# Optimization experiments

Hardware: AMD Instinct MI355X
Metric: run time of the kernel (lower is better)

Reference implementation:

```python
import jax, jax.numpy as jnp
import numpy as np

PAD_IDX = 1
BATCH = 16
TLEN = 128
SLEN = 400          # full source length
AGENDA_LEN = 100    # slen_ in src_map
CONTEXT_LEN = SLEN - AGENDA_LEN
INPUT_SIZE = 1024
VOCAB = 32000
CVOCAB = 120


def setup_inputs() -> dict:
    key = jax.random.key(0)
    k1, k2, k3, k4, k5, k6, k7 = jax.random.split(key, 7)
    N = BATCH * TLEN
    hidden = jax.random.normal(k1, (N, INPUT_SIZE), dtype=jnp.float32)
    attn = jax.random.uniform(k2, (N, SLEN), dtype=jnp.float32)
    attn = attn / jnp.sum(attn, axis=1, keepdims=True)  # attention-like rows
    src_map = jax.random.uniform(k3, (AGENDA_LEN, BATCH, CVOCAB), dtype=jnp.float32)
    W = jax.random.normal(k4, (VOCAB, INPUT_SIZE), dtype=jnp.float32) * 0.02
    b = jnp.zeros((VOCAB,), dtype=jnp.float32)
    W_copy = jax.random.normal(k5, (1, INPUT_SIZE), dtype=jnp.float32) * 0.02
    b_copy = jnp.zeros((1,), dtype=jnp.float32)
    return {"hidden": hidden, "attn": attn, "src_map": src_map,
            "W": W, "b": b, "W_copy": W_copy, "b_copy": b_copy}


def reference(hidden, attn, src_map, W, b, W_copy, b_copy):
    # hidden: (tlen*batch, d), attn: (tlen*batch, slen), src_map: (agenda, batch, cvocab)
    agenda_len, batch, cvocab = src_map.shape
    slen = attn.shape[1]
    context_len = slen - agenda_len

    logits = hidden @ W.T + b                       # (N, vocab)
    logits = logits.at[:, PAD_IDX].set(-jnp.inf)
    prob = jax.nn.softmax(logits, axis=1)
    p_copy = jax.nn.sigmoid(hidden @ W_copy.T + b_copy)  # (N, 1)

    out_prob = prob * (1.0 - p_copy)                # (N, vocab)
    mul_attn = attn[:, context_len:] * p_copy       # (N, agenda)

    # rows are ordered (tlen, batch); bmm against per-batch indicator map
    ma = mul_attn.reshape(-1, batch, agenda_len)    # (tlen, batch, agenda)
    copy_prob = jnp.einsum('tba,abv->tbv', ma, src_map)  # (tlen, batch, cvocab)
    copy_prob = copy_prob.reshape(-1, cvocab)       # (N, cvocab)

    return jnp.concatenate([out_prob, copy_prob], axis=1), p_copy
```

## Files before the change

kernel.cpp:

```cpp
#include <hip/hip_runtime.h>

#define M_DIM 2048
#define K_DIM 1024
#define N_DIM 32000
#define CVOCAB 120
#define AGENDA 100
#define SLEN 400
#define CTX 300
#define BATCH 16
#define OUT_STRIDE 32120
#define PAD_IDX 1

#define TM 256
#define TN 256
#define BK 64

typedef float f32x4_t  __attribute__((ext_vector_type(4)));
typedef __bf16 bf16x8_t __attribute__((ext_vector_type(8)));
typedef unsigned short u16x8_t __attribute__((ext_vector_type(8)));
typedef unsigned short u16x4_t __attribute__((ext_vector_type(4)));

__device__ __forceinline__ unsigned short f2bf(float f) {
    union { float f; unsigned int u; } c; c.f = f;
    unsigned int u = c.u;
    u += 0x7FFFu + ((u >> 16) & 1u);
    return (unsigned short)(u >> 16);
}

__device__ __forceinline__ void async_copy16(const void* gsrc, void* ldst) {
    __builtin_amdgcn_global_load_lds(
        (__attribute__((address_space(1))) unsigned int*)(gsrc),
        (__attribute__((address_space(3))) unsigned int*)(ldst),
        16, 0, 0);
}

__global__ void cast_bf16_kernel(const float4* __restrict__ W, const float4* __restrict__ H,
                                 unsigned short* __restrict__ Wb, unsigned short* __restrict__ Hb) {
    const size_t NW4 = (size_t)N_DIM * K_DIM / 4;
    const size_t NH4 = (size_t)M_DIM * K_DIM / 4;
    size_t idx = (size_t)blockIdx.x * 256 + threadIdx.x;
    float4 v; unsigned short* dst;
    if (idx < NW4)            { v = W[idx];        dst = Wb + idx * 4; }
    else if (idx < NW4 + NH4) { v = H[idx - NW4];  dst = Hb + (idx - NW4) * 4; }
    else return;
    u16x4_t o;
    o[0] = f2bf(v.x); o[1] = f2bf(v.y); o[2] = f2bf(v.z); o[3] = f2bf(v.w);
    *(u16x4_t*)dst = o;
}

__global__ void pcopy_kernel(const float* __restrict__ hidden, const float* __restrict__ Wc,
                             const float* __restrict__ bc, float* __restrict__ pcopy) {
    int row  = blockIdx.x * 4 + (threadIdx.x >> 6);
    int lane = threadIdx.x & 63;
    const float4* h = (const float4*)(hidden + (size_t)row * K_DIM);
    const float4* w = (const float4*)Wc;
    float s = 0.f;
    #pragma unroll
    for (int i = 0; i < 4; ++i) {
        float4 a = h[lane + 64 * i];
        float4 b = w[lane + 64 * i];
        s += a.x * b.x + a.y * b.y + a.z * b.z + a.w * b.w;
    }
    #pragma unroll
    for (int m = 1; m < 64; m <<= 1) s += __shfl_xor(s, m);
    if (lane == 0) {
        float p = 1.0f / (1.0f + __expf(-(s + bc[0])));
        pcopy[row] = p;
    }
}

__global__ __launch_bounds__(1024, 4) void gemm_exp_kernel(
    const unsigned short* __restrict__ A,
    const unsigned short* __restrict__ B,
    const float* __restrict__ bias,
    float* __restrict__ out,
    float* __restrict__ rowsum)
{
    __shared__ unsigned short sA[TM * BK];
    __shared__ unsigned short sB[TN * BK];
    __shared__ float sRow[TM];

    const int tid   = threadIdx.x;
    const int lane  = tid & 63;
    const int q     = lane >> 4;
    const int lr    = lane & 15;
    const int wv    = tid >> 6;
    const int waveM = wv >> 2;
    const int waveN = wv & 3;
    const int rowBase = blockIdx.x * TM;
    const int colBase = blockIdx.y * TN;

    f32x4_t acc[4][4] = {};

    if (tid < TM) sRow[tid] = 0.0f;

    const unsigned short* aSrc[2];
    const unsigned short* bSrc[2];
    unsigned short* aDst[2];
    unsigned short* bDst[2];
    #pragma unroll
    for (int it = 0; it < 2; ++it) {
        int p = it * 1024 + tid;
        int m = p >> 3;
        int j = (p & 7) ^ (m & 7);
        aSrc[it] = A + (size_t)(rowBase + m) * K_DIM + j * 8;
        bSrc[it] = B + (size_t)(colBase + m) * K_DIM + j * 8;
        aDst[it] = sA + (it * 1024 + (tid & ~63)) * 8;
        bDst[it] = sB + (it * 1024 + (tid & ~63)) * 8;
    }

    for (int k0 = 0; k0 < K_DIM; k0 += BK) {
        #pragma unroll
        for (int it = 0; it < 2; ++it) async_copy16(aSrc[it] + k0, aDst[it]);
        #pragma unroll
        for (int it = 0; it < 2; ++it) async_copy16(bSrc[it] + k0, bDst[it]);
        __syncthreads();

        #pragma unroll
        for (int s = 0; s < 2; ++s) {
            u16x8_t af[4], bfr[4];
            #pragma unroll
            for (int r = 0; r < 4; ++r) {
                int m  = waveM * 64 + r * 16 + lr;
                int ch = (s * 4 + q) ^ (m & 7);
                af[r] = *(const u16x8_t*)(sA + m * BK + ch * 8);
            }
            #pragma unroll
            for (int c = 0; c < 4; ++c) {
                int n  = waveN * 64 + c * 16 + lr;
                int ch = (s * 4 + q) ^ (n & 7);
                bfr[c] = *(const u16x8_t*)(sB + n * BK + ch * 8);
            }
            #pragma unroll
            for (int r = 0; r < 4; ++r)
                #pragma unroll
                for (int c = 0; c < 4; ++c)
                    acc[r][c] = __builtin_amdgcn_mfma_f32_16x16x32_bf16(
                        __builtin_bit_cast(bf16x8_t, af[r]),
                        __builtin_bit_cast(bf16x8_t, bfr[c]),
                        acc[r][c], 0, 0, 0);
        }
        __syncthreads();
    }

    float bb[4];
    #pragma unroll
    for (int c = 0; c < 4; ++c) bb[c] = bias[colBase + waveN * 64 + c * 16 + lr];

    #pragma unroll
    for (int r = 0; r < 4; ++r) {
        float rsum[4] = {0.f, 0.f, 0.f, 0.f};
        #pragma unroll
        for (int c = 0; c < 4; ++c) {
            int gcol = colBase + waveN * 64 + c * 16 + lr;
            #pragma unroll
            for (int d = 0; d < 4; ++d) {
                int grow = rowBase + waveM * 64 + r * 16 + q * 4 + d;
                float e = (gcol == PAD_IDX) ? 0.0f : __expf(acc[r][c][d] + bb[c]);
                out[(size_t)grow * OUT_STRIDE + gcol] = e;
                rsum[d] += e;
            }
        }
        #pragma unroll
        for (int d = 0; d < 4; ++d) {
            float v = rsum[d];
            v += __shfl_xor(v, 1);
            v += __shfl_xor(v, 2);
            v += __shfl_xor(v, 4);
            v += __shfl_xor(v, 8);
            if (lr == 0) {
                int lrow = waveM * 64 + r * 16 + q * 4 + d;
                atomicAdd(&sRow[lrow], v);
            }
        }
    }
    __syncthreads();
    if (tid < TM) atomicAdd(&rowsum[rowBase + tid], sRow[tid]);
}

__global__ void finalize_kernel(float* __restrict__ out, const float* __restrict__ rowsum,
                                const float* __restrict__ pcopy, const float* __restrict__ attn,
                                const float* __restrict__ src_map, float* __restrict__ out_tail) {
    int n   = blockIdx.x;
    int tid = threadIdx.x;
    int bidx = n & (BATCH - 1);
    float p = pcopy[n];
    float scale = (1.0f - p) / rowsum[n];

    __shared__ float ma[AGENDA];
    if (tid < AGENDA) ma[tid] = attn[(size_t)n * SLEN + CTX + tid] * p;

    float4* row4 = (float4*)(out + (size_t)n * OUT_STRIDE);
    for (int j = tid; j < N_DIM / 4; j += 256) {
        float4 v = row4[j];
        v.x *= scale; v.y *= scale; v.z *= scale; v.w *= scale;
        row4[j] = v;
    }
    __syncthreads();

    if (tid < CVOCAB) {
        float s = 0.f;
        #pragma unroll 4
        for (int a = 0; a < AGENDA; ++a)
            s += ma[a] * src_map[(size_t)(a * BATCH + bidx) * CVOCAB + tid];
        out[(size_t)n * OUT_STRIDE + N_DIM + tid] = s;
    }
    if (tid == 0) out_tail[n] = p;
}

extern "C" void kernel_launch(void* const* d_in, const int* in_sizes, int n_in,
                              void* d_out, int out_size, void* d_ws, size_t ws_size,
                              hipStream_t stream) {
    const float* hidden  = (const float*)d_in[0];
    const float* attn    = (const float*)d_in[1];
    const float* src_map = (const float*)d_in[2];
    const float* W       = (const float*)d_in[3];
    const float* b       = (const float*)d_in[4];
    const float* W_copy  = (const float*)d_in[5];
    const float* b_copy  = (const float*)d_in[6];
    float* out = (float*)d_out;

    char* ws = (char*)d_ws;
    unsigned short* Wb = (unsigned short*)ws;
    unsigned short* Hb = (unsigned short*)(ws + 65536000);
    float* rowsum      = (float*)(ws + 65536000 + 4194304);
    float* pcopy       = (float*)(ws + 65536000 + 4194304 + 8192);

    float* out_tail = out + (size_t)M_DIM * OUT_STRIDE;

    {
        size_t total4 = (size_t)N_DIM * K_DIM / 4 + (size_t)M_DIM * K_DIM / 4;
        int blocks = (int)((total4 + 255) / 256);
        cast_bf16_kernel<<<blocks, 256, 0, stream>>>((const float4*)W, (const float4*)hidden, Wb, Hb);
    }
    hipMemsetAsync(rowsum, 0, M_DIM * sizeof(float), stream);
    pcopy_kernel<<<M_DIM / 4, 256, 0, stream>>>(hidden, W_copy, b_copy, pcopy);
    {
        dim3 grid(M_DIM / TM, N_DIM / TN);
        gemm_exp_kernel<<<grid, 1024, 0, stream>>>(Hb, Wb, b, out, rowsum);
    }
    finalize_kernel<<<M_DIM, 256, 0, stream>>>(out, rowsum, pcopy, attn, src_map, out_tail);
}
```

Baseline: 625.2 us.

## Double-buffer GEMM LDS, remap block order, stage exp values as fp16 in place

Double-buffers the LDS tiles so the next K tile's async loads overlap the current MFMA work. Linearizes the grid and remaps block IDs so consecutive blocks share W column tiles for L2 reuse. The GEMM epilogue writes exp values as fp16 into the first half of each output row, and finalize copies that half-row into LDS before expanding and scaling it back to fp32. This halves the intermediate write traffic. Rowsum zeroing moves into pcopy_kernel to drop the memset. Risks: fp16 overflow or precision loss for large exp values, and the in-place staging depends on a whole-row LDS copy before any overwrite.

```diff
diff --git a/kernel.cpp b/kernel.cpp
--- a/kernel.cpp
+++ b/kernel.cpp
@@ -14,6 +14,10 @@
 #define TM 256
 #define TN 256
 #define BK 64
+#define BUFSZ (TM * BK)
+#define NKT (K_DIM / BK)
+#define MT (M_DIM / TM)
+#define NT (N_DIM / TN)
 
 typedef float f32x4_t  __attribute__((ext_vector_type(4)));
 typedef __bf16 bf16x8_t __attribute__((ext_vector_type(8)));
@@ -25,6 +29,14 @@
     unsigned int u = c.u;
     u += 0x7FFFu + ((u >> 16) & 1u);
     return (unsigned short)(u >> 16);
+}
+
+__device__ __forceinline__ unsigned short f2h(float f) {
+    _Float16 h = (_Float16)f;
+    unsigned short u; __builtin_memcpy(&u, &h, 2); return u;
+}
+__device__ __forceinline__ float h2f(unsigned short u) {
+    _Float16 h; __builtin_memcpy(&h, &u, 2); return (float)h;
 }
 
 __device__ __forceinline__ void async_copy16(const void* gsrc, void* ldst) {
@@ -49,7 +61,8 @@
 }
 
 __global__ void pcopy_kernel(const float* __restrict__ hidden, const float* __restrict__ Wc,
-                             const float* __restrict__ bc, float* __restrict__ pcopy) {
+                             const float* __restrict__ bc, float* __restrict__ pcopy,
+                             float* __restrict__ rowsum) {
     int row  = blockIdx.x * 4 + (threadIdx.x >> 6);
     int lane = threadIdx.x & 63;
     const float4* h = (const float4*)(hidden + (size_t)row * K_DIM);
@@ -66,6 +79,7 @@
     if (lane == 0) {
         float p = 1.0f / (1.0f + __expf(-(s + bc[0])));
         pcopy[row] = p;
+        rowsum[row] = 0.0f;
     }
 }
 
@@ -76,8 +90,8 @@
     float* __restrict__ out,
     float* __restrict__ rowsum)
 {
-    __shared__ unsigned short sA[TM * BK];
-    __shared__ unsigned short sB[TN * BK];
+    __shared__ unsigned short sA[2][BUFSZ];
+    __shared__ unsigned short sB[2][BUFSZ];
     __shared__ float sRow[TM];
 
     const int tid   = threadIdx.x;
@@ -87,35 +101,42 @@
     const int wv    = tid >> 6;
     const int waveM = wv >> 2;
     const int waveN = wv & 3;
-    const int rowBase = blockIdx.x * TM;
-    const int colBase = blockIdx.y * TN;
+
+    const int bid = blockIdx.x;
+    const int t   = (bid & 7) * NT + (bid >> 3);
+    const int rowBase = (t & 7) * TM;
+    const int colBase = (t >> 3) * TN;
 
     f32x4_t acc[4][4] = {};
-
     if (tid < TM) sRow[tid] = 0.0f;
 
-    const unsigned short* aSrc[2];
-    const unsigned short* bSrc[2];
-    unsigned short* aDst[2];
-    unsigned short* bDst[2];
-    #pragma unroll
-    for (int it = 0; it < 2; ++it) {
-        int p = it * 1024 + tid;
-        int m = p >> 3;
-        int j = (p & 7) ^ (m & 7);
-        aSrc[it] = A + (size_t)(rowBase + m) * K_DIM + j * 8;
-        bSrc[it] = B + (size_t)(colBase + m) * K_DIM + j * 8;
-        aDst[it] = sA + (it * 1024 + (tid & ~63)) * 8;
-        bDst[it] = sB + (it * 1024 + (tid & ~63)) * 8;
-    }
-
-    for (int k0 = 0; k0 < K_DIM; k0 += BK) {
-        #pragma unroll
-        for (int it = 0; it < 2; ++it) async_copy16(aSrc[it] + k0, aDst[it]);
-        #pragma unroll
-        for (int it = 0; it < 2; ++it) async_copy16(bSrc[it] + k0, bDst[it]);
-        __syncthreads();
-
+    const int p0 = tid,        m0 = p0 >> 3, j0 = (p0 & 7) ^ (m0 & 7);
+    const int p1 = 1024 + tid, m1 = p1 >> 3, j1 = (p1 & 7) ^ (m1 & 7);
+    const unsigned short* aSrc0 = A + (size_t)(rowBase + m0) * K_DIM + j0 * 8;
+    const unsigned short* aSrc1 = A + (size_t)(rowBase + m1) * K_DIM + j1 * 8;
+    const unsigned short* bSrc0 = B + (size_t)(colBase + m0) * K_DIM + j0 * 8;
+    const unsigned short* bSrc1 = B + (size_t)(colBase + m1) * K_DIM + j1 * 8;
+    const int dOff0 = (tid & ~63) * 8;
+    const int dOff1 = (1024 + (tid & ~63)) * 8;
+
+    async_copy16(aSrc0, &sA[0][dOff0]);
+    async_copy16(aSrc1, &sA[0][dOff1]);
+    async_copy16(bSrc0, &sB[0][dOff0]);
+    async_copy16(bSrc1, &sB[0][dOff1]);
+    __syncthreads();
+
+    for (int kt = 0; kt < NKT; ++kt) {
+        const int cur = kt & 1;
+        if (kt + 1 < NKT) {
+            const int nb = cur ^ 1;
+            const int k0 = (kt + 1) * BK;
+            async_copy16(aSrc0 + k0, &sA[nb][dOff0]);
+            async_copy16(aSrc1 + k0, &sA[nb][dOff1]);
+            async_copy16(bSrc0 + k0, &sB[nb][dOff0]);
+            async_copy16(bSrc1 + k0, &sB[nb][dOff1]);
+        }
+        const unsigned short* pA = sA[cur];
+        const unsigned short* pB = sB[cur];
         #pragma unroll
         for (int s = 0; s < 2; ++s) {
             u16x8_t af[4], bfr[4];
@@ -123,13 +144,13 @@
             for (int r = 0; r < 4; ++r) {
                 int m  = waveM * 64 + r * 16 + lr;
                 int ch = (s * 4 + q) ^ (m & 7);
-                af[r] = *(const u16x8_t*)(sA + m * BK + ch * 8);
+                af[r] = *(const u16x8_t*)(pA + m * BK + ch * 8);
             }
             #pragma unroll
             for (int c = 0; c < 4; ++c) {
                 int n  = waveN * 64 + c * 16 + lr;
                 int ch = (s * 4 + q) ^ (n & 7);
-                bfr[c] = *(const u16x8_t*)(sB + n * BK + ch * 8);
+                bfr[c] = *(const u16x8_t*)(pB + n * BK + ch * 8);
             }
             #pragma unroll
             for (int r = 0; r < 4; ++r)
@@ -153,11 +174,12 @@
         #pragma unroll
         for (int c = 0; c < 4; ++c) {
             int gcol = colBase + waveN * 64 + c * 16 + lr;
+            bool pad = (gcol == PAD_IDX);
             #pragma unroll
             for (int d = 0; d < 4; ++d) {
                 int grow = rowBase + waveM * 64 + r * 16 + q * 4 + d;
-                float e = (gcol == PAD_IDX) ? 0.0f : __expf(acc[r][c][d] + bb[c]);
-                out[(size_t)grow * OUT_STRIDE + gcol] = e;
+                float e = pad ? 0.0f : __expf(acc[r][c][d] + bb[c]);
+                ((unsigned short*)(out + (size_t)grow * OUT_STRIDE))[gcol] = f2h(e);
                 rsum[d] += e;
             }
         }
@@ -178,27 +200,37 @@
     if (tid < TM) atomicAdd(&rowsum[rowBase + tid], sRow[tid]);
 }
 
-__global__ void finalize_kernel(float* __restrict__ out, const float* __restrict__ rowsum,
-                                const float* __restrict__ pcopy, const float* __restrict__ attn,
-                                const float* __restrict__ src_map, float* __restrict__ out_tail) {
-    int n   = blockIdx.x;
-    int tid = threadIdx.x;
-    int bidx = n & (BATCH - 1);
-    float p = pcopy[n];
-    float scale = (1.0f - p) / rowsum[n];
-
+__global__ __launch_bounds__(512) void finalize_kernel(
+    float* __restrict__ out, const float* __restrict__ rowsum,
+    const float* __restrict__ pcopy, const float* __restrict__ attn,
+    const float* __restrict__ src_map, float* __restrict__ out_tail) {
+    const int n   = blockIdx.x;
+    const int tid = threadIdx.x;
+    __shared__ unsigned short sE[N_DIM];
     __shared__ float ma[AGENDA];
+
+    const float p = pcopy[n];
+    const float scale = (1.0f - p) / rowsum[n];
+
+    const u16x8_t* src = (const u16x8_t*)(out + (size_t)n * OUT_STRIDE);
+    for (int j = tid; j < N_DIM / 8; j += 512)
+        *(u16x8_t*)(sE + j * 8) = src[j];
     if (tid < AGENDA) ma[tid] = attn[(size_t)n * SLEN + CTX + tid] * p;
+    __syncthreads();
 
     float4* row4 = (float4*)(out + (size_t)n * OUT_STRIDE);
-    for (int j = tid; j < N_DIM / 4; j += 256) {
-        float4 v = row4[j];
-        v.x *= scale; v.y *= scale; v.z *= scale; v.w *= scale;
+    for (int j = tid; j < N_DIM / 4; j += 512) {
+        u16x4_t h = *(const u16x4_t*)(sE + j * 4);
+        float4 v;
+        v.x = h2f(h[0]) * scale;
+        v.y = h2f(h[1]) * scale;
+        v.z = h2f(h[2]) * scale;
+        v.w = h2f(h[3]) * scale;
         row4[j] = v;
     }
-    __syncthreads();
 
     if (tid < CVOCAB) {
+        int bidx = n & (BATCH - 1);
         float s = 0.f;
         #pragma unroll 4
         for (int a = 0; a < AGENDA; ++a)
@@ -233,11 +265,7 @@
         int blocks = (int)((total4 + 255) / 256);
         cast_bf16_kernel<<<blocks, 256, 0, stream>>>((const float4*)W, (const float4*)hidden, Wb, Hb);
     }
-    hipMemsetAsync(rowsum, 0, M_DIM * sizeof(float), stream);
-    pcopy_kernel<<<M_DIM / 4, 256, 0, stream>>>(hidden, W_copy, b_copy, pcopy);
-    {
-        dim3 grid(M_DIM / TM, N_DIM / TN);
-        gemm_exp_kernel<<<grid, 1024, 0, stream>>>(Hb, Wb, b, out, rowsum);
-    }
-    finalize_kernel<<<M_DIM, 256, 0, stream>>>(out, rowsum, pcopy, attn, src_map, out_tail);
-}
+    pcopy_kernel<<<M_DIM / 4, 256, 0, stream>>>(hidden, W_copy, b_copy, pcopy, rowsum);
+    gemm_exp_kernel<<<MT * NT, 1024, 0, stream>>>(Hb, Wb, b, out, rowsum);
+    finalize_kernel<<<M_DIM, 512, 0, stream>>>(out, rowsum, pcopy, attn, src_map, out_tail);
+}
```

Result: faster. 582.8 us (-6.8%).
